# Optimization experiments

Measured on AMD Instinct MI355X. Metric: run time of the kernel, lower is better.

Reference implementation:

```python
import jax, jax.numpy as jnp
import numpy as np

D_MODEL = 768
D_STATE = 16
D_CONV = 4
EXPAND = 2
D_INNER = EXPAND * D_MODEL  # 1536
DT_RANK = 48  # ceil(768/16)
D_FF = 3072
EPS = 1e-5


def layer_norm(x, g, b):
    mu = jnp.mean(x, axis=-1, keepdims=True)
    var = jnp.mean((x - mu) ** 2, axis=-1, keepdims=True)
    return (x - mu) * jax.lax.rsqrt(var + EPS) * g + b


def selective_scan(u, delta, A, Bm, Cm, Dp, delta_bias):
    # u, delta: (B, d, L); A: (d, n); Bm, Cm: (B, n, L); Dp: (d,)
    delta = jax.nn.softplus(delta + delta_bias[None, :, None])
    dT = jnp.moveaxis(delta, 2, 0)  # (L, B, d)
    uT = jnp.moveaxis(u, 2, 0)      # (L, B, d)
    BT = jnp.moveaxis(Bm, 2, 0)     # (L, B, n)
    CT = jnp.moveaxis(Cm, 2, 0)     # (L, B, n)

    def step(h, inp):
        d_t, u_t, b_t, c_t = inp
        dA = jnp.exp(d_t[:, :, None] * A)                      # (B, d, n)
        h = dA * h + (d_t * u_t)[:, :, None] * b_t[:, None, :]  # (B, d, n)
        y = jnp.einsum('bdn,bn->bd', h, c_t)
        return h, y

    h0 = jnp.zeros((u.shape[0], A.shape[0], A.shape[1]), u.dtype)
    _, ys = jax.lax.scan(step, h0, (dT, uT, BT, CT))  # ys: (L, B, d)
    y = jnp.moveaxis(ys, 0, 2)  # (B, d, L)
    return y + u * Dp[None, :, None]


def mamba_mixer(x, in_proj_w, conv_w, conv_b, x_proj_w, dt_proj_w, dt_proj_b,
                A_log, D_param, out_proj_w):
    # x: (B, L, d_model)
    B, L, _ = x.shape
    x_and_res = x @ in_proj_w.T                      # (B, L, 2*d_inner)
    xs, res = jnp.split(x_and_res, [D_INNER], axis=-1)
    xi = jnp.transpose(xs, (0, 2, 1))                # (B, d_inner, L)
    # causal depthwise conv (torch pads d_conv-1 both sides then slices [:L])
    xi = jax.lax.conv_general_dilated(
        xi, conv_w, window_strides=(1,), padding=[(D_CONV - 1, 0)],
        feature_group_count=D_INNER,
        dimension_numbers=('NCH', 'OIH', 'NCH')) + conv_b[None, :, None]
    xs = jax.nn.silu(jnp.transpose(xi, (0, 2, 1)))   # (B, L, d_inner)
    # SSM
    proj = xs @ x_proj_w.T                           # (B, L, dt_rank + 2n)
    dt, Bm, Cm = jnp.split(proj, [DT_RANK, DT_RANK + D_STATE], axis=-1)
    delta = jnp.einsum('blr,dr->bdl', dt, dt_proj_w)  # (B, d_inner, L)
    A = -jnp.exp(A_log)                               # (d_inner, n)
    y = selective_scan(jnp.transpose(xs, (0, 2, 1)), delta, A,
                       jnp.transpose(Bm, (0, 2, 1)), jnp.transpose(Cm, (0, 2, 1)),
                       D_param, dt_proj_b)            # (B, d_inner, L)
    y = jnp.transpose(y, (0, 2, 1)) * jax.nn.silu(res)
    return y @ out_proj_w.T                           # (B, L, d_model)


def setup_inputs() -> dict:
    key = jax.random.key(0)
    ks = jax.random.split(key, 16)
    s = 0.02
    src = jax.random.normal(ks[0], (4, 8, 128, D_MODEL), jnp.float32)
    in_proj_w = jax.random.normal(ks[1], (2 * D_INNER, D_MODEL), jnp.float32) * s
    conv_w = jax.random.normal(ks[2], (D_INNER, 1, D_CONV), jnp.float32) * 0.2
    conv_b = jnp.zeros((D_INNER,), jnp.float32)
    x_proj_w = jax.random.normal(ks[3], (DT_RANK + 2 * D_STATE, D_INNER), jnp.float32) * s
    dt_std = DT_RANK ** -0.5
    dt_proj_w = jax.random.uniform(ks[4], (D_INNER, DT_RANK), jnp.float32, -dt_std, dt_std)
    dt = jnp.exp(jax.random.uniform(ks[5], (D_INNER,), jnp.float32) *
                 (np.log(0.1) - np.log(0.001)) + np.log(0.001))
    dt = jnp.clip(dt, 1e-4, None)
    dt_proj_b = dt + jnp.log(-jnp.expm1(-dt))
    A_log = jnp.log(jnp.broadcast_to(jnp.arange(1, D_STATE + 1, dtype=jnp.float32),
                                     (D_INNER, D_STATE)))
    D_param = jnp.ones((D_INNER,), jnp.float32)
    out_proj_w = jax.random.normal(ks[6], (D_MODEL, D_INNER), jnp.float32) * s
    return {
        'src': src,
        'norm1_g': jnp.ones((D_MODEL,), jnp.float32), 'norm1_b': jnp.zeros((D_MODEL,), jnp.float32),
        'in_proj_w': in_proj_w, 'conv_w': conv_w, 'conv_b': conv_b,
        'x_proj_w': x_proj_w, 'dt_proj_w': dt_proj_w, 'dt_proj_b': dt_proj_b,
        'A_log': A_log, 'D_param': D_param, 'out_proj_w': out_proj_w,
        'norm2_g': jnp.ones((D_MODEL,), jnp.float32), 'norm2_b': jnp.zeros((D_MODEL,), jnp.float32),
        'w1': jax.random.normal(ks[7], (D_FF, D_MODEL), jnp.float32) * s,
        'b1': jnp.zeros((D_FF,), jnp.float32),
        'w2': jax.random.normal(ks[8], (D_MODEL, D_FF), jnp.float32) * s,
        'b2': jnp.zeros((D_MODEL,), jnp.float32),
    }


def reference(src, norm1_g, norm1_b, in_proj_w, conv_w, conv_b, x_proj_w,
              dt_proj_w, dt_proj_b, A_log, D_param, out_proj_w,
              norm2_g, norm2_b, w1, b1, w2, b2):
    Bz, Ch, P, Dm = src.shape
    x = src
    # pre-norm mixer block (dropout=0 / eval)
    h = layer_norm(x, norm1_g, norm1_b).reshape(Bz, Ch * P, Dm)
    m = mamba_mixer(h, in_proj_w, conv_w, conv_b, x_proj_w, dt_proj_w,
                    dt_proj_b, A_log, D_param, out_proj_w).reshape(Bz, Ch, P, Dm)
    x = x + m
    # pre-norm FFN block (exact GELU like torch F.gelu default)
    h2 = layer_norm(x, norm2_g, norm2_b)
    ff = jax.nn.gelu(h2 @ w1.T + b1, approximate=False) @ w2.T + b2
    return x + ff
```

## Files before the change

kernel.cpp:

```cpp
#include <hip/hip_runtime.h>
#include <cstdint>
#include <cstddef>

typedef __attribute__((ext_vector_type(4))) float f32x4;
typedef __attribute__((ext_vector_type(8))) short s16x8;

#if __has_builtin(__builtin_amdgcn_exp2f)
#define EXP2F(x) __builtin_amdgcn_exp2f(x)
#else
#define EXP2F(x) __expf((x) * 0.6931471805599453f)
#endif
#if __has_builtin(__builtin_amdgcn_rcpf)
#define RCPF(x) __builtin_amdgcn_rcpf(x)
#else
#define RCPF(x) (1.0f / (x))
#endif

__device__ inline unsigned short f2b(float f) {
  union { float f; unsigned u; } c; c.f = f;
  return (unsigned short)((c.u + 0x7FFFu + ((c.u >> 16) & 1u)) >> 16);
}
__device__ inline float b2f(unsigned short u) {
  union { unsigned u; float f; } c; c.u = ((unsigned)u) << 16;
  return c.f;
}

__device__ inline void gload_lds16(const void* g, void* l) {
  __builtin_amdgcn_global_load_lds(
      (const __attribute__((address_space(1))) unsigned int*)g,
      (__attribute__((address_space(3))) unsigned int*)l, 16, 0, 0);
}

#define RAW_BARRIER() asm volatile("s_barrier" ::: "memory")

__global__ __launch_bounds__(256) void cvt_all(const float* __restrict__ inW,
                                               const float* __restrict__ outW,
                                               const float* __restrict__ w1,
                                               const float* __restrict__ w2,
                                               unsigned short* __restrict__ wbA,
                                               unsigned short* __restrict__ wbO,
                                               unsigned short* __restrict__ wb1,
                                               unsigned short* __restrict__ wb2) {
  int i = blockIdx.x * 256 + threadIdx.x;
  const float* src;
  unsigned short* dst;
  int o;
  if (i < 589824)       { src = inW;  dst = wbA; o = i; }
  else if (i < 884736)  { src = outW; dst = wbO; o = i - 589824; }
  else if (i < 1474560) { src = w1;   dst = wb1; o = i - 884736; }
  else                  { src = w2;   dst = wb2; o = i - 1474560; }
  float4 v = ((const float4*)src)[o];
  ushort4 u;
  u.x = f2b(v.x); u.y = f2b(v.y); u.z = f2b(v.z); u.w = f2b(v.w);
  ((ushort4*)dst)[o] = u;
}

__global__ __launch_bounds__(256) void build_proj(const float* __restrict__ xpw,
                                                  const float* __restrict__ dtw,
                                                  unsigned short* __restrict__ wpad,
                                                  unsigned short* __restrict__ wdt) {
  int i = blockIdx.x * 256 + threadIdx.x;
  if (i < 196608) {
    int row = i / 1536;
    wpad[i] = (row < 80) ? f2b(xpw[i]) : (unsigned short)0;
  } else {
    int j = i - 196608;
    int row = j >> 6, k = j & 63;
    wdt[j] = (k < 48) ? f2b(dtw[row * 48 + k]) : (unsigned short)0;
  }
}

__global__ __launch_bounds__(256) void reduce_projA(const float* __restrict__ Pa,
                                                    unsigned short* __restrict__ dtbf,
                                                    float* __restrict__ projBC) {
  int i = blockIdx.x * 256 + threadIdx.x;
  int row = i >> 7, col = i & 127;
  float s = Pa[i] + Pa[i + 524288] + Pa[i + 1048576] + Pa[i + 1572864];
  if (col < 48) {
    dtbf[row * 64 + col] = f2b(s);
  } else if (col < 64) {
    dtbf[row * 64 + col] = 0;
    projBC[row * 32 + col - 48] = s;
  } else if (col < 80) {
    projBC[row * 32 + col - 48] = s;
  }
}

__global__ __launch_bounds__(256) void ln_kernel(const float* __restrict__ x,
                                                 const float* __restrict__ gam,
                                                 const float* __restrict__ bet,
                                                 unsigned short* __restrict__ out) {
  int w = threadIdx.x >> 6, lane = threadIdx.x & 63;
  size_t row = (size_t)blockIdx.x * 4 + w;
  const float4* xr = (const float4*)(x + row * 768);
  float4 v0 = xr[lane], v1 = xr[lane + 64], v2 = xr[lane + 128];
  float s = v0.x + v0.y + v0.z + v0.w + v1.x + v1.y + v1.z + v1.w +
            v2.x + v2.y + v2.z + v2.w;
  #pragma unroll
  for (int o = 32; o; o >>= 1) s += __shfl_xor(s, o);
  float mu = s * (1.f / 768.f);
  float q = 0.f;
  {
    float d;
    d = v0.x - mu; q += d * d; d = v0.y - mu; q += d * d;
    d = v0.z - mu; q += d * d; d = v0.w - mu; q += d * d;
    d = v1.x - mu; q += d * d; d = v1.y - mu; q += d * d;
    d = v1.z - mu; q += d * d; d = v1.w - mu; q += d * d;
    d = v2.x - mu; q += d * d; d = v2.y - mu; q += d * d;
    d = v2.z - mu; q += d * d; d = v2.w - mu; q += d * d;
  }
  #pragma unroll
  for (int o = 32; o; o >>= 1) q += __shfl_xor(q, o);
  float rs = rsqrtf(q * (1.f / 768.f) + 1e-5f);
  const float4* gr = (const float4*)gam;
  const float4* br = (const float4*)bet;
  ushort4* orow = (ushort4*)(out + row * 768);
  float4 vv[3] = {v0, v1, v2};
  #pragma unroll
  for (int i = 0; i < 3; ++i) {
    int c4 = lane + i * 64;
    float4 g4 = gr[c4], b4 = br[c4];
    ushort4 o;
    o.x = f2b((vv[i].x - mu) * rs * g4.x + b4.x);
    o.y = f2b((vv[i].y - mu) * rs * g4.y + b4.y);
    o.z = f2b((vv[i].z - mu) * rs * g4.z + b4.z);
    o.w = f2b((vv[i].w - mu) * rs * g4.w + b4.w);
    orow[c4] = o;
  }
}

__global__ __launch_bounds__(256) void reduce_ln(
    const unsigned short* __restrict__ Pp, const float* __restrict__ src,
    const float* __restrict__ gam, const float* __restrict__ bet,
    float* __restrict__ xbuf, unsigned short* __restrict__ hbf) {
  int w = threadIdx.x >> 6, lane = threadIdx.x & 63;
  size_t row = (size_t)blockIdx.x * 4 + w;
  const float4* s4 = (const float4*)(src + row * 768);
  const ushort4* p0 = (const ushort4*)(Pp + row * 768);
  const ushort4* p1 = (const ushort4*)(Pp + 3145728 + row * 768);
  float4* xb4 = (float4*)(xbuf + row * 768);
  float4 xv[3];
  float s = 0.f;
  #pragma unroll
  for (int j = 0; j < 3; ++j) {
    int c4 = lane + j * 64;
    float4 a = s4[c4];
    ushort4 b = p0[c4], c = p1[c4];
    float4 x;
    x.x = a.x + b2f(b.x) + b2f(c.x); x.y = a.y + b2f(b.y) + b2f(c.y);
    x.z = a.z + b2f(b.z) + b2f(c.z); x.w = a.w + b2f(b.w) + b2f(c.w);
    xv[j] = x;
    xb4[c4] = x;
    s += x.x + x.y + x.z + x.w;
  }
  #pragma unroll
  for (int o = 32; o; o >>= 1) s += __shfl_xor(s, o);
  float mu = s * (1.f / 768.f);
  float q = 0.f;
  #pragma unroll
  for (int j = 0; j < 3; ++j) {
    float d;
    d = xv[j].x - mu; q += d * d; d = xv[j].y - mu; q += d * d;
    d = xv[j].z - mu; q += d * d; d = xv[j].w - mu; q += d * d;
  }
  #pragma unroll
  for (int o = 32; o; o >>= 1) q += __shfl_xor(q, o);
  float rs = rsqrtf(q * (1.f / 768.f) + 1e-5f);
  const float4* gr = (const float4*)gam;
  const float4* br = (const float4*)bet;
  ushort4* orow = (ushort4*)(hbf + row * 768);
  #pragma unroll
  for (int j = 0; j < 3; ++j) {
    int c4 = lane + j * 64;
    float4 g4 = gr[c4], b4 = br[c4];
    ushort4 o;
    o.x = f2b((xv[j].x - mu) * rs * g4.x + b4.x);
    o.y = f2b((xv[j].y - mu) * rs * g4.y + b4.y);
    o.z = f2b((xv[j].z - mu) * rs * g4.z + b4.z);
    o.w = f2b((xv[j].w - mu) * rs * g4.w + b4.w);
    orow[c4] = o;
  }
}

__global__ __launch_bounds__(256) void reduce_out(
    const unsigned short* __restrict__ Pp, const float* __restrict__ xbuf,
    const float* __restrict__ bias, float* __restrict__ outp) {
  int i = blockIdx.x * 256 + threadIdx.x;
  int r = i / 192;
  int c4 = i - r * 192;
  float4 b4 = ((const float4*)bias)[c4];
  float4 x = ((const float4*)xbuf)[i];
  ushort4 p0 = ((const ushort4*)Pp)[i];
  ushort4 p1 = ((const ushort4*)(Pp + 3145728))[i];
  float4 o;
  o.x = x.x + b4.x + b2f(p0.x) + b2f(p1.x);
  o.y = x.y + b4.y + b2f(p0.y) + b2f(p1.y);
  o.z = x.z + b4.z + b2f(p0.z) + b2f(p1.z);
  o.w = x.w + b4.w + b2f(p0.w) + b2f(p1.w);
  ((float4*)outp)[i] = o;
}

__global__ __launch_bounds__(256) void conv_silu(const unsigned short* __restrict__ xs_pre,
                                                 const float* __restrict__ cw,
                                                 const float* __restrict__ cb,
                                                 unsigned short* __restrict__ xs_act) {
  int idx = blockIdx.x * 256 + threadIdx.x;
  int t = idx / 384;
  int c4 = idx - t * 384;
  int pos = t & 1023;
  const unsigned short* base = xs_pre + (size_t)t * 1536 + c4 * 4;
  ushort4 z = {0, 0, 0, 0};
  ushort4 x3 = *(const ushort4*)base;
  ushort4 x2 = (pos >= 1) ? *(const ushort4*)(base - 1536) : z;
  ushort4 x1 = (pos >= 2) ? *(const ushort4*)(base - 3072) : z;
  ushort4 x0 = (pos >= 3) ? *(const ushort4*)(base - 4608) : z;
  float a0[4] = {b2f(x0.x), b2f(x0.y), b2f(x0.z), b2f(x0.w)};
  float a1[4] = {b2f(x1.x), b2f(x1.y), b2f(x1.z), b2f(x1.w)};
  float a2[4] = {b2f(x2.x), b2f(x2.y), b2f(x2.z), b2f(x2.w)};
  float a3[4] = {b2f(x3.x), b2f(x3.y), b2f(x3.z), b2f(x3.w)};
  ushort4 o;
  unsigned short* op = &o.x;
  #pragma unroll
  for (int i = 0; i < 4; ++i) {
    int dd = c4 * 4 + i;
    float4 wv = *(const float4*)(cw + dd * 4);
    float v = wv.x * a0[i] + wv.y * a1[i] + wv.z * a2[i] + wv.w * a3[i] + cb[dd];
    float sv = v * RCPF(1.f + __expf(-v));
    op[i] = f2b(sv);
  }
  *(ushort4*)(xs_act + (size_t)t * 1536 + c4 * 4) = o;
}

__global__ __launch_bounds__(256) void scan_p1(
    const unsigned short* __restrict__ dsp, const unsigned short* __restrict__ u_bf,
    const float* __restrict__ projBC, const float* __restrict__ A_log,
    float* __restrict__ Pbuf, float* __restrict__ Hbuf) {
  int tid = threadIdx.x;
  int dl = tid >> 1;
  int nh = (tid & 1) * 8;
  int blk = blockIdx.x;
  int c = blk & 31;
  int bt = blk >> 5;
  int b = bt / 12;
  int dtile = bt - b * 12;
  int d = dtile * 128 + dl;
  float Al2[8];
  {
    float4 a0 = *(const float4*)(A_log + d * 16 + nh);
    float4 a1 = *(const float4*)(A_log + d * 16 + nh + 4);
    const float L2E = 1.4426950408889634f;
    Al2[0] = -__expf(a0.x) * L2E; Al2[1] = -__expf(a0.y) * L2E;
    Al2[2] = -__expf(a0.z) * L2E; Al2[3] = -__expf(a0.w) * L2E;
    Al2[4] = -__expf(a1.x) * L2E; Al2[5] = -__expf(a1.y) * L2E;
    Al2[6] = -__expf(a1.z) * L2E; Al2[7] = -__expf(a1.w) * L2E;
  }
  const unsigned short* base_d = dsp + (size_t)b * 1024 * 1536 + d;
  const float* base_bc = projBC + (size_t)b * 1024 * 32 + nh;
  const unsigned short* ub = u_bf + (size_t)b * 1024 * 1536 + d;
  float h[8];
  #pragma unroll
  for (int k = 0; k < 8; ++k) h[k] = 0.f;
  float S = 0.f;
  int t0 = c * 32;
  float dspA = b2f(base_d[(size_t)t0 * 1536]);
  float utA = b2f(ub[(size_t)t0 * 1536]);
  float4 B0A = *(const float4*)(base_bc + (size_t)t0 * 32);
  float4 B1A = *(const float4*)(base_bc + (size_t)t0 * 32 + 4);
  float dspB, utB;
  float4 B0B, B1B;
#define P1_BODY(DSP, UT, B0, B1)                                   \
  {                                                                \
    S += DSP;                                                      \
    float du = DSP * UT;                                           \
    float Bv[8] = {B0.x, B0.y, B0.z, B0.w, B1.x, B1.y, B1.z, B1.w};\
    _Pragma("unroll")                                              \
    for (int k = 0; k < 8; ++k) {                                  \
      float dA = EXP2F(DSP * Al2[k]);                              \
      h[k] = __builtin_fmaf(dA, h[k], du * Bv[k]);                 \
    }                                                              \
  }
  for (int s = 0; s < 32; s += 2) {
    size_t t1 = t0 + s + 1;
    dspB = b2f(base_d[t1 * 1536]);
    utB = b2f(ub[t1 * 1536]);
    B0B = *(const float4*)(base_bc + t1 * 32);
    B1B = *(const float4*)(base_bc + t1 * 32 + 4);
    P1_BODY(dspA, utA, B0A, B1A);
    int t2i = t0 + s + 2; if (t2i > 1023) t2i = 1023;
    size_t t2 = t2i;
    dspA = b2f(base_d[t2 * 1536]);
    utA = b2f(ub[t2 * 1536]);
    B0A = *(const float4*)(base_bc + t2 * 32);
    B1A = *(const float4*)(base_bc + t2 * 32 + 4);
    P1_BODY(dspB, utB, B0B, B1B);
  }
#undef P1_BODY
  int j = c * 98304 + (b * 1536 + d) * 16 + nh;
  float4 P0 = make_float4(EXP2F(Al2[0] * S), EXP2F(Al2[1] * S),
                          EXP2F(Al2[2] * S), EXP2F(Al2[3] * S));
  float4 P1 = make_float4(EXP2F(Al2[4] * S), EXP2F(Al2[5] * S),
                          EXP2F(Al2[6] * S), EXP2F(Al2[7] * S));
  *(float4*)(Pbuf + j) = P0;
  *(float4*)(Pbuf + j + 4) = P1;
  *(float4*)(Hbuf + j) = make_float4(h[0], h[1], h[2], h[3]);
  *(float4*)(Hbuf + j + 4) = make_float4(h[4], h[5], h[6], h[7]);
}

__global__ __launch_bounds__(256) void scan_p2(float* __restrict__ Pbuf,
                                               const float* __restrict__ Hbuf) {
  int i = blockIdx.x * 256 + threadIdx.x;
  float H = 0.f;
  #pragma unroll
  for (int c = 0; c < 32; ++c) {
    int j = c * 98304 + i;
    float P = Pbuf[j];
    float he = Hbuf[j];
    Pbuf[j] = H;
    H = __builtin_fmaf(P, H, he);
  }
}

__global__ __launch_bounds__(256) void scan_p3(
    const unsigned short* __restrict__ dsp, const unsigned short* __restrict__ u_bf,
    const float* __restrict__ projBC, const unsigned short* __restrict__ res_pre,
    const float* __restrict__ A_log, const float* __restrict__ D_param,
    const float* __restrict__ Pbuf, unsigned short* __restrict__ y_out) {
  int tid = threadIdx.x;
  int dl = tid >> 1;
  int nh = (tid & 1) * 8;
  int blk = blockIdx.x;
  int c = blk & 31;
  int bt = blk >> 5;
  int b = bt / 12;
  int dtile = bt - b * 12;
  int d = dtile * 128 + dl;
  float Dp = D_param[d];
  float Al2[8];
  {
    float4 a0 = *(const float4*)(A_log + d * 16 + nh);
    float4 a1 = *(const float4*)(A_log + d * 16 + nh + 4);
    const float L2E = 1.4426950408889634f;
    Al2[0] = -__expf(a0.x) * L2E; Al2[1] = -__expf(a0.y) * L2E;
    Al2[2] = -__expf(a0.z) * L2E; Al2[3] = -__expf(a0.w) * L2E;
    Al2[4] = -__expf(a1.x) * L2E; Al2[5] = -__expf(a1.y) * L2E;
    Al2[6] = -__expf(a1.z) * L2E; Al2[7] = -__expf(a1.w) * L2E;
  }
  const unsigned short* base_d = dsp + (size_t)b * 1024 * 1536 + d;
  const float* base_bc = projBC + (size_t)b * 1024 * 32 + nh;
  const unsigned short* ub = u_bf + (size_t)b * 1024 * 1536 + d;
  const unsigned short* rbase = res_pre + (size_t)b * 1024 * 1536 + d;
  unsigned short* yrow = y_out + (size_t)b * 1024 * 1536 + d;
  int j = c * 98304 + (b * 1536 + d) * 16 + nh;
  float h[8];
  {
    float4 h0 = *(const float4*)(Pbuf + j);
    float4 h1 = *(const float4*)(Pbuf + j + 4);
    h[0] = h0.x; h[1] = h0.y; h[2] = h0.z; h[3] = h0.w;
    h[4] = h1.x; h[5] = h1.y; h[6] = h1.z; h[7] = h1.w;
  }
  int t0 = c * 32;
  float dspA = b2f(base_d[(size_t)t0 * 1536]);
  float utA = b2f(ub[(size_t)t0 * 1536]);
  float4 B0A = *(const float4*)(base_bc + (size_t)t0 * 32);
  float4 B1A = *(const float4*)(base_bc + (size_t)t0 * 32 + 4);
  float4 C0A = *(const float4*)(base_bc + (size_t)t0 * 32 + 16);
  float4 C1A = *(const float4*)(base_bc + (size_t)t0 * 32 + 20);
  float rA = b2f(rbase[(size_t)t0 * 1536]);
  float dspB, utB, rB;
  float4 B0B, B1B, C0B, C1B;
#define P3_BODY(DSP, UT, B0, B1, C0, C1, RV, TT)                   \
  {                                                                \
    float du = DSP * UT;                                           \
    float Bv[8] = {B0.x, B0.y, B0.z, B0.w, B1.x, B1.y, B1.z, B1.w};\
    float Cv[8] = {C0.x, C0.y, C0.z, C0.w, C1.x, C1.y, C1.z, C1.w};\
    float p0 = 0.f, p1v = 0.f;                                     \
    _Pragma("unroll")                                              \
    for (int k = 0; k < 8; ++k) {                                  \
      float dA = EXP2F(DSP * Al2[k]);                              \
      h[k] = __builtin_fmaf(dA, h[k], du * Bv[k]);                 \
      if (k & 1) p1v = __builtin_fmaf(h[k], Cv[k], p1v);           \
      else       p0  = __builtin_fmaf(h[k], Cv[k], p0);            \
    }                                                              \
    float p = p0 + p1v;                                            \
    p += __int_as_float(__builtin_amdgcn_update_dpp(               \
        0, __float_as_int(p), 0xB1, 0xF, 0xF, true));              \
    if (nh == 0) {                                                 \
      float sr = RV * RCPF(1.f + __expf(-RV));                     \
      yrow[(size_t)(TT) * 1536] = f2b(__builtin_fmaf(UT, Dp, p) * sr); \
    }                                                              \
  }
  for (int s = 0; s < 32; s += 2) {
    size_t t1 = t0 + s + 1;
    dspB = b2f(base_d[t1 * 1536]);
    utB = b2f(ub[t1 * 1536]);
    B0B = *(const float4*)(base_bc + t1 * 32);
    B1B = *(const float4*)(base_bc + t1 * 32 + 4);
    C0B = *(const float4*)(base_bc + t1 * 32 + 16);
    C1B = *(const float4*)(base_bc + t1 * 32 + 20);
    rB = b2f(rbase[t1 * 1536]);
    P3_BODY(dspA, utA, B0A, B1A, C0A, C1A, rA, t0 + s);
    int t2i = t0 + s + 2; if (t2i > 1023) t2i = 1023;
    size_t t2 = t2i;
    dspA = b2f(base_d[t2 * 1536]);
    utA = b2f(ub[t2 * 1536]);
    B0A = *(const float4*)(base_bc + t2 * 32);
    B1A = *(const float4*)(base_bc + t2 * 32 + 4);
    C0A = *(const float4*)(base_bc + t2 * 32 + 16);
    C1A = *(const float4*)(base_bc + t2 * 32 + 20);
    rA = b2f(rbase[t2 * 1536]);
    P3_BODY(dspB, utB, B0B, B1B, C0B, C1B, rB, t1);
  }
#undef P3_BODY
}

template <int MODE, int BM>
__global__ __launch_bounds__(256, 2) void gemm_bt(
    const unsigned short* __restrict__ A, const unsigned short* __restrict__ B,
    int M, int N, int K, float* __restrict__ Cf, unsigned short* __restrict__ Cb,
    const float* __restrict__ res, const float* __restrict__ bias) {
  constexpr int NFR = (BM == 128) ? 4 : 2;
  constexpr int AIT = BM / 64;
  constexpr int NB  = (BM == 128) ? 3 : 4;
  __shared__ __align__(16) unsigned short As[NB][BM * 32];
  __shared__ __align__(16) unsigned short Bs[NB][128 * 32];
  int tid = threadIdx.x;
  int lane = tid & 63;
  int w = tid >> 6;
  int wm = (BM == 128) ? (w >> 1) : 0;
  int wn = (BM == 128) ? (w & 1) : w;
  int row0 = blockIdx.x * BM;
  int col0 = blockIdx.y * 128;
  const int lr = lane & 15;
  const int kb = lane >> 4;
  int ksl = K / gridDim.z;
  int kbeg = blockIdx.z * ksl;

  f32x4 acc[4][NFR];
  #pragma unroll
  for (int i = 0; i < 4; ++i)
    #pragma unroll
    for (int j = 0; j < NFR; ++j) acc[i][j] = (f32x4)0.f;

  auto stage = [&](int buf, int k0) {
    #pragma unroll
    for (int j = 0; j < AIT; ++j) {
      int e = j * 256 + tid;
      int r = e >> 2, cc = e & 3;
      int sc = cc ^ ((r >> 1) & 3);
      gload_lds16(A + (size_t)(row0 + r) * K + k0 + sc * 8, &As[buf][e * 8]);
    }
    #pragma unroll
    for (int j = 0; j < 2; ++j) {
      int e = j * 256 + tid;
      int r = e >> 2, cc = e & 3;
      int sc = cc ^ ((r >> 1) & 3);
      gload_lds16(B + (size_t)(col0 + r) * K + k0 + sc * 8, &Bs[buf][e * 8]);
    }
  };

  int nt = ksl >> 5;
  stage(0, kbeg);
  if (nt > 1) stage(1, kbeg + 32);
  if (NB > 2 && nt > 2) stage(2, kbeg + 64);
  if (NB > 3 && nt > 3) stage(3, kbeg + 96);

  int cur = 0;
  for (int t = 0; t < nt; ++t) {
    int rem = nt - 1 - t;
    if (NB == 4) {
      if (rem >= 3)      asm volatile("s_waitcnt vmcnt(9)" ::: "memory");
      else if (rem == 2) asm volatile("s_waitcnt vmcnt(6)" ::: "memory");
      else if (rem == 1) asm volatile("s_waitcnt vmcnt(3)" ::: "memory");
      else               asm volatile("s_waitcnt vmcnt(0)" ::: "memory");
    } else {
      if (rem >= 2)      asm volatile("s_waitcnt vmcnt(8)" ::: "memory");
      else if (rem == 1) asm volatile("s_waitcnt vmcnt(4)" ::: "memory");
      else               asm volatile("s_waitcnt vmcnt(0)" ::: "memory");
    }
    RAW_BARRIER();
    s16x8 af[4], bfm[NFR];
    #pragma unroll
    for (int m = 0; m < 4; ++m) {
      int rr = wm * 64 + m * 16 + lr;
      int chunk = rr * 4 + (kb ^ ((rr >> 1) & 3));
      af[m] = *(const s16x8*)&As[cur][chunk * 8];
    }
    #pragma unroll
    for (int nn = 0; nn < NFR; ++nn) {
      int rr = wn * (16 * NFR) + nn * 16 + lr;
      int chunk = rr * 4 + (kb ^ ((rr >> 1) & 3));
      bfm[nn] = *(const s16x8*)&Bs[cur][chunk * 8];
    }
    #pragma unroll
    for (int m = 0; m < 4; ++m)
      #pragma unroll
      for (int nn = 0; nn < NFR; ++nn)
        acc[m][nn] = __builtin_amdgcn_mfma_f32_16x16x32_bf16(af[m], bfm[nn], acc[m][nn], 0, 0, 0);
    RAW_BARRIER();
    if (t + NB < nt) stage(cur, kbeg + ((t + NB) << 5));
    cur = (cur + 1 == NB) ? 0 : cur + 1;
  }

  size_t zoff = (size_t)blockIdx.z * M * N;
  #pragma unroll
  for (int m = 0; m < 4; ++m) {
    int rbase = row0 + wm * 64 + m * 16 + kb * 4;
    #pragma unroll
    for (int nn = 0; nn < NFR; ++nn) {
      int col = col0 + wn * (16 * NFR) + nn * 16 + lr;
      #pragma unroll
      for (int r = 0; r < 4; ++r) {
        int row = rbase + r;
        size_t idx = (size_t)row * N + col;
        float v = acc[m][nn][r];
        if (MODE == 2) {
          float tt = v + bias[col];
          float gl = 0.5f * tt * (1.f + erff(tt * 0.7071067811865475f));
          Cb[idx] = f2b(gl);
        } else if (MODE == 5) {
          Cf[zoff + idx] = v;
        } else if (MODE == 6) {
          float xx = v + bias[col];
          float sp = (xx > 20.f) ? xx : __logf(1.f + __expf(xx));
          Cb[idx] = f2b(sp);
        } else if (MODE == 7) {
          if (col < 1536) {
            Cb[(size_t)row * 1536 + col] = f2b(v);
          } else {
            ((unsigned short*)Cf)[(size_t)row * 1536 + col - 1536] = f2b(v);
          }
        } else {
          Cb[zoff + idx] = f2b(v);
        }
      }
    }
  }
}

extern "C" void kernel_launch(void* const* d_in, const int* in_sizes, int n_in,
                              void* d_out, int out_size, void* d_ws, size_t ws_size,
                              hipStream_t stream) {
  (void)in_sizes; (void)n_in; (void)out_size; (void)ws_size;
  const float* src   = (const float*)d_in[0];
  const float* n1g   = (const float*)d_in[1];
  const float* n1b   = (const float*)d_in[2];
  const float* inW   = (const float*)d_in[3];
  const float* convW = (const float*)d_in[4];
  const float* convB = (const float*)d_in[5];
  const float* xpW   = (const float*)d_in[6];
  const float* dtW   = (const float*)d_in[7];
  const float* dtB   = (const float*)d_in[8];
  const float* Alog  = (const float*)d_in[9];
  const float* Dpar  = (const float*)d_in[10];
  const float* outW  = (const float*)d_in[11];
  const float* n2g   = (const float*)d_in[12];
  const float* n2b   = (const float*)d_in[13];
  const float* w1    = (const float*)d_in[14];
  const float* b1    = (const float*)d_in[15];
  const float* w2    = (const float*)d_in[16];
  const float* b2    = (const float*)d_in[17];

  char* ws = (char*)d_ws;
  unsigned short* wbA   = (unsigned short*)(ws + 0);
  unsigned short* wbO   = (unsigned short*)(ws + 4718592);
  unsigned short* wb1   = (unsigned short*)(ws + 7077888);
  unsigned short* wb2   = (unsigned short*)(ws + 11796480);
  unsigned short* wpad  = (unsigned short*)(ws + 16515072);
  unsigned short* wdt   = (unsigned short*)(ws + 16908288);
  unsigned short* hbf   = (unsigned short*)(ws + 21626880);
  unsigned short* xs_pre= (unsigned short*)(ws + 27918336);
  unsigned short* res_pre=(unsigned short*)(ws + 40501248);
  float*          Pbuf  = (float*)(ws + 53084160);
  float*          Hbuf  = (float*)(ws + 65667072);
  unsigned short* Ppbh  = (unsigned short*)(ws + 53084160);
  unsigned short* xsact = (unsigned short*)(ws + 78249984);
  float*          xbuf  = (float*)(ws + 78249984);
  unsigned short* dsp   = (unsigned short*)(ws + 90832896);
  unsigned short* ff1   = (unsigned short*)(ws + 90832896);
  float*          projBC= (float*)(ws + 115998720);
  unsigned short* dtbf  = (unsigned short*)(ws + 116523008);
  float*          Pa    = (float*)(ws + 118095872);
  unsigned short* ybuf  = (unsigned short*)(ws + 118095872);
  float* outp = (float*)d_out;

  cvt_all<<<8064, 256, 0, stream>>>(inW, outW, w1, w2, wbA, wbO, wb1, wb2);
  build_proj<<<1152, 256, 0, stream>>>(xpW, dtW, wpad, wdt);

  ln_kernel<<<1024, 256, 0, stream>>>(src, n1g, n1b, hbf);
  gemm_bt<7, 128><<<dim3(32, 24), 256, 0, stream>>>(hbf, wbA, 4096, 3072, 768, (float*)res_pre, xs_pre, nullptr, nullptr);
  conv_silu<<<6144, 256, 0, stream>>>(xs_pre, convW, convB, xsact);

  gemm_bt<5, 64><<<dim3(64, 1, 4), 256, 0, stream>>>(xsact, wpad, 4096, 128, 1536, Pa, nullptr, nullptr, nullptr);
  reduce_projA<<<2048, 256, 0, stream>>>(Pa, dtbf, projBC);
  gemm_bt<6, 128><<<dim3(32, 12), 256, 0, stream>>>(dtbf, wdt, 4096, 1536, 64, nullptr, dsp, nullptr, dtB);

  scan_p1<<<1536, 256, 0, stream>>>(dsp, xsact, projBC, Alog, Pbuf, Hbuf);
  scan_p2<<<384, 256, 0, stream>>>(Pbuf, Hbuf);
  scan_p3<<<1536, 256, 0, stream>>>(dsp, xsact, projBC, res_pre, Alog, Dpar, Pbuf, ybuf);

  gemm_bt<8, 64><<<dim3(64, 6, 2), 256, 0, stream>>>(ybuf, wbO, 4096, 768, 1536, nullptr, Ppbh, nullptr, nullptr);
  reduce_ln<<<1024, 256, 0, stream>>>(Ppbh, src, n2g, n2b, xbuf, hbf);

  gemm_bt<2, 128><<<dim3(32, 24), 256, 0, stream>>>(hbf, wb1, 4096, 3072, 768, nullptr, ff1, nullptr, b1);
  gemm_bt<8, 64><<<dim3(64, 6, 2), 256, 0, stream>>>(ff1, wb2, 4096, 768, 3072, nullptr, Ppbh, nullptr, nullptr);
  reduce_out<<<3072, 256, 0, stream>>>(Ppbh, xbuf, b2, outp);
}
```

Measured before the change: 252.1 us.

## Stage GEMM epilogue through LDS for vector stores; use split-K 4 with 128-row tiles

The bf16 GEMM epilogue now writes accumulators into swizzled LDS (reusing the A/B staging buffers) and then emits coalesced 16-byte row stores, replacing scattered 2-byte global writes. The out-proj and FFN2 GEMMs switch from 64-row tiles with split-K of 2 to 128-row tiles with split-K of 4. The reduce kernels now sum four partial slices instead of two. This trades more partial-sum traffic and reduction work for better store coalescing and larger tiles. The epilogue reuse of LDS relies on prior barriers and assumes 64-column warp tiles.

```diff
diff --git a/kernel.cpp b/kernel.cpp
--- a/kernel.cpp
+++ b/kernel.cpp
@@ -138,6 +138,8 @@
   const float4* s4 = (const float4*)(src + row * 768);
   const ushort4* p0 = (const ushort4*)(Pp + row * 768);
   const ushort4* p1 = (const ushort4*)(Pp + 3145728 + row * 768);
+  const ushort4* p2 = (const ushort4*)(Pp + 6291456 + row * 768);
+  const ushort4* p3 = (const ushort4*)(Pp + 9437184 + row * 768);
   float4* xb4 = (float4*)(xbuf + row * 768);
   float4 xv[3];
   float s = 0.f;
@@ -145,10 +147,12 @@
   for (int j = 0; j < 3; ++j) {
     int c4 = lane + j * 64;
     float4 a = s4[c4];
-    ushort4 b = p0[c4], c = p1[c4];
+    ushort4 b = p0[c4], c = p1[c4], d2 = p2[c4], e = p3[c4];
     float4 x;
-    x.x = a.x + b2f(b.x) + b2f(c.x); x.y = a.y + b2f(b.y) + b2f(c.y);
-    x.z = a.z + b2f(b.z) + b2f(c.z); x.w = a.w + b2f(b.w) + b2f(c.w);
+    x.x = a.x + b2f(b.x) + b2f(c.x) + b2f(d2.x) + b2f(e.x);
+    x.y = a.y + b2f(b.y) + b2f(c.y) + b2f(d2.y) + b2f(e.y);
+    x.z = a.z + b2f(b.z) + b2f(c.z) + b2f(d2.z) + b2f(e.z);
+    x.w = a.w + b2f(b.w) + b2f(c.w) + b2f(d2.w) + b2f(e.w);
     xv[j] = x;
     xb4[c4] = x;
     s += x.x + x.y + x.z + x.w;
@@ -192,11 +196,13 @@
   float4 x = ((const float4*)xbuf)[i];
   ushort4 p0 = ((const ushort4*)Pp)[i];
   ushort4 p1 = ((const ushort4*)(Pp + 3145728))[i];
+  ushort4 p2 = ((const ushort4*)(Pp + 6291456))[i];
+  ushort4 p3 = ((const ushort4*)(Pp + 9437184))[i];
   float4 o;
-  o.x = x.x + b4.x + b2f(p0.x) + b2f(p1.x);
-  o.y = x.y + b4.y + b2f(p0.y) + b2f(p1.y);
-  o.z = x.z + b4.z + b2f(p0.z) + b2f(p1.z);
-  o.w = x.w + b4.w + b2f(p0.w) + b2f(p1.w);
+  o.x = x.x + b4.x + b2f(p0.x) + b2f(p1.x) + b2f(p2.x) + b2f(p3.x);
+  o.y = x.y + b4.y + b2f(p0.y) + b2f(p1.y) + b2f(p2.y) + b2f(p3.y);
+  o.z = x.z + b4.z + b2f(p0.z) + b2f(p1.z) + b2f(p2.z) + b2f(p3.z);
+  o.w = x.w + b4.w + b2f(p0.w) + b2f(p1.w) + b2f(p2.w) + b2f(p3.w);
   ((float4*)outp)[i] = o;
 }
 
@@ -502,37 +508,66 @@
   }
 
   size_t zoff = (size_t)blockIdx.z * M * N;
-  #pragma unroll
-  for (int m = 0; m < 4; ++m) {
-    int rbase = row0 + wm * 64 + m * 16 + kb * 4;
-    #pragma unroll
-    for (int nn = 0; nn < NFR; ++nn) {
-      int col = col0 + wn * (16 * NFR) + nn * 16 + lr;
+  if constexpr (MODE == 5) {
+    #pragma unroll
+    for (int m = 0; m < 4; ++m) {
+      int rbase = row0 + wm * 64 + m * 16 + kb * 4;
       #pragma unroll
-      for (int r = 0; r < 4; ++r) {
-        int row = rbase + r;
-        size_t idx = (size_t)row * N + col;
-        float v = acc[m][nn][r];
-        if (MODE == 2) {
-          float tt = v + bias[col];
-          float gl = 0.5f * tt * (1.f + erff(tt * 0.7071067811865475f));
-          Cb[idx] = f2b(gl);
-        } else if (MODE == 5) {
-          Cf[zoff + idx] = v;
-        } else if (MODE == 6) {
-          float xx = v + bias[col];
-          float sp = (xx > 20.f) ? xx : __logf(1.f + __expf(xx));
-          Cb[idx] = f2b(sp);
-        } else if (MODE == 7) {
-          if (col < 1536) {
-            Cb[(size_t)row * 1536 + col] = f2b(v);
-          } else {
-            ((unsigned short*)Cf)[(size_t)row * 1536 + col - 1536] = f2b(v);
-          }
-        } else {
-          Cb[zoff + idx] = f2b(v);
+      for (int nn = 0; nn < NFR; ++nn) {
+        int col = col0 + wn * (16 * NFR) + nn * 16 + lr;
+        #pragma unroll
+        for (int r = 0; r < 4; ++r) {
+          Cf[zoff + (size_t)(rbase + r) * N + col] = acc[m][nn][r];
         }
       }
+    }
+  } else {
+    unsigned short* ep = (w < NB) ? (unsigned short*)&As[w][0]
+                                  : (unsigned short*)&Bs[w - NB][0];
+    #pragma unroll
+    for (int m = 0; m < 4; ++m) {
+      #pragma unroll
+      for (int nn = 0; nn < NFR; ++nn) {
+        int cl = nn * 16 + lr;
+        #pragma unroll
+        for (int r = 0; r < 4; ++r) {
+          int rl = m * 16 + kb * 4 + r;
+          float v = acc[m][nn][r];
+          float o;
+          if (MODE == 2) {
+            float tt = v + bias[col0 + wn * 64 + cl];
+            o = 0.5f * tt * (1.f + erff(tt * 0.7071067811865475f));
+          } else if (MODE == 6) {
+            float xx = v + bias[col0 + wn * 64 + cl];
+            o = (xx > 20.f) ? xx : __logf(1.f + __expf(xx));
+          } else {
+            o = v;
+          }
+          ep[rl * 64 + (cl ^ ((rl & 7) << 3))] = f2b(o);
+        }
+      }
+    }
+    asm volatile("s_waitcnt lgkmcnt(0)" ::: "memory");
+    int colbase = col0 + wn * 64;
+    unsigned short* dst;
+    size_t rstride;
+    int cb2 = colbase;
+    if (MODE == 7) {
+      rstride = 1536;
+      if (colbase < 1536) dst = Cb;
+      else { dst = (unsigned short*)Cf; cb2 = colbase - 1536; }
+    } else if (MODE == 8) {
+      dst = Cb + zoff; rstride = N;
+    } else {
+      dst = Cb; rstride = N;
+    }
+    int rowb = row0 + wm * 64;
+    #pragma unroll
+    for (int i = 0; i < 8; ++i) {
+      int rl = i * 8 + (lane >> 3);
+      int cl = (lane & 7) * 8;
+      s16x8 vv = *(const s16x8*)&ep[rl * 64 + (cl ^ ((rl & 7) << 3))];
+      *(s16x8*)(dst + (size_t)(rowb + rl) * rstride + cb2 + cl) = vv;
     }
   }
 }
@@ -598,10 +633,10 @@
   scan_p2<<<384, 256, 0, stream>>>(Pbuf, Hbuf);
   scan_p3<<<1536, 256, 0, stream>>>(dsp, xsact, projBC, res_pre, Alog, Dpar, Pbuf, ybuf);
 
-  gemm_bt<8, 64><<<dim3(64, 6, 2), 256, 0, stream>>>(ybuf, wbO, 4096, 768, 1536, nullptr, Ppbh, nullptr, nullptr);
+  gemm_bt<8, 128><<<dim3(32, 6, 4), 256, 0, stream>>>(ybuf, wbO, 4096, 768, 1536, nullptr, Ppbh, nullptr, nullptr);
   reduce_ln<<<1024, 256, 0, stream>>>(Ppbh, src, n2g, n2b, xbuf, hbf);
 
   gemm_bt<2, 128><<<dim3(32, 24), 256, 0, stream>>>(hbf, wb1, 4096, 3072, 768, nullptr, ff1, nullptr, b1);
-  gemm_bt<8, 64><<<dim3(64, 6, 2), 256, 0, stream>>>(ff1, wb2, 4096, 768, 3072, nullptr, Ppbh, nullptr, nullptr);
+  gemm_bt<8, 128><<<dim3(32, 6, 4), 256, 0, stream>>>(ff1, wb2, 4096, 768, 3072, nullptr, Ppbh, nullptr, nullptr);
   reduce_out<<<3072, 256, 0, stream>>>(Ppbh, xbuf, b2, outp);
 }
```

New measurement: 247.0 us. 1.02x faster.
